# Kernel optimization log

Measured on AMD Instinct MI355X. Metric: run time of the kernel, lower is better.

The kernel has to match this reference:

```python
import jax, jax.numpy as jnp
import numpy as np
from jax import lax

H = 256  # hidden_dim
NDIM = 3
K = 32   # k_neighbors


def sincos_embed(coords, dim, ndim):
    # ContinuousSinCosEmbed: per-coordinate sin/cos features, zero-padded to `dim`.
    dpn = dim // ndim          # channels per coordinate
    half = dpn // 2
    freqs = 1.0 / (10000.0 ** (jnp.arange(half, dtype=coords.dtype) / half))
    ang = coords[..., :, None] * freqs                      # (..., ndim, half)
    emb = jnp.concatenate([jnp.sin(ang), jnp.cos(ang)], -1)  # (..., ndim, 2*half)
    emb = emb.reshape(coords.shape[:-1] + (ndim * 2 * half,))
    pad = dim - ndim * 2 * half
    if pad:
        emb = jnp.concatenate([emb, jnp.zeros(emb.shape[:-1] + (pad,), emb.dtype)], -1)
    return emb


def setup_inputs() -> dict:
    key = jax.random.key(0)
    ks = jax.random.split(key, 8)
    N, S = 50000, 1024
    positions = jax.random.uniform(ks[0], (N, NDIM), dtype=jnp.float32) * 10.0
    supernode_indices = jax.random.randint(ks[1], (S,), 0, N, dtype=jnp.int32)
    g = 1.0 / np.sqrt(H)
    W1 = jax.random.normal(ks[2], (H, H), jnp.float32) * g
    b1 = jnp.zeros((H,), jnp.float32)
    W2 = jax.random.normal(ks[3], (H, H), jnp.float32) * g
    b2 = jnp.zeros((H,), jnp.float32)
    Wp = jax.random.normal(ks[4], (2 * H, H), jnp.float32) * (1.0 / np.sqrt(2 * H))
    bp = jnp.zeros((H,), jnp.float32)
    return {"positions": positions, "supernode_indices": supernode_indices,
            "W1": W1, "b1": b1, "W2": W2, "b2": b2, "Wp": Wp, "bp": bp}


def reference(positions, supernode_indices, W1, b1, W2, b2, Wp, bp):
    # positions: (N, 3); supernode_indices: (S,)
    sup_pos = positions[supernode_indices]                 # (S, 3)
    # kNN neighbor search via dense pairwise squared distances (memory-bound)
    diff = sup_pos[:, None, :] - positions[None, :, :]     # (S, N, 3)
    dist2 = jnp.sum(diff * diff, axis=-1)                  # (S, N)
    _, nbr_idx = lax.top_k(-dist2, K)                      # (S, K)
    nbr_pos = positions[nbr_idx]                           # (S, K, 3)
    # relpos mode: embed (relative position, distance) -> ndim+1 = 4 coords
    rel = sup_pos[:, None, :] - nbr_pos                    # (S, K, 3)
    d = jnp.sqrt(jnp.sum(rel * rel, axis=-1, keepdims=True))  # (S, K, 1)
    rel_feat = jnp.concatenate([rel, d], axis=-1)          # (S, K, 4)
    msg_in = sincos_embed(rel_feat, H, NDIM + 1)           # (S, K, H)
    # message MLP: Dense -> gelu -> Dense
    h = jax.nn.gelu(jnp.einsum('ski,ij->skj', msg_in, W1) + b1)
    msgs = jnp.einsum('ski,ij->skj', h, W2) + b2           # (S, K, H)
    # scatter-reduce: mean over neighbors per supernode
    agg = jnp.mean(msgs, axis=1)                           # (S, H)
    # supernode absolute position embedding, concat, project
    sup_emb = sincos_embed(sup_pos, H, NDIM)               # (S, H)
    feats = jnp.concatenate([sup_emb, agg], axis=-1)       # (S, 2H)
    out = feats @ Wp + bp                                  # (S, H)
    return out[None]                                        # (1, S, H)
```

## Files before the change

### kernel.cpp

```cpp
#include <hip/hip_runtime.h>
#include <hip/hip_bf16.h>
#include <math.h>

typedef short bf16x8 __attribute__((ext_vector_type(8)));
typedef float f32x4  __attribute__((ext_vector_type(4)));

constexpr int   H     = 256;
constexpr int   KNB   = 32;
constexpr int   GC    = 16;
constexpr float HINV  = 1.6f;
constexpr float HCEL  = 0.625f;
constexpr int   SLOTS = 32;
constexpr int   OCAP  = 256;
constexpr int   CAP   = 512;

__device__ __forceinline__ ushort f2bf(float x) {
    unsigned u = __float_as_uint(x);
    u += 0x7FFF + ((u >> 16) & 1);
    return (ushort)(u >> 16);
}

__device__ __forceinline__ float gelu_fast(float x) {
    float u = 0.7978845608028654f * (x + 0.044715f * x * x * x);
    float t = exp2f(-2.885390081777927f * u);
    return x / (1.0f + t);
}

__device__ __forceinline__ int cell_of(float x, float y, float z) {
    int cx = min(GC - 1, max(0, (int)(x * HINV)));
    int cy = min(GC - 1, max(0, (int)(y * HINV)));
    int cz = min(GC - 1, max(0, (int)(z * HINV)));
    return (cz * GC + cy) * GC + cx;
}

__global__ __launch_bounds__(256)
void prep(const float* __restrict__ W1, const float* __restrict__ pos, int N,
          ushort* __restrict__ W1t, float4* __restrict__ pos4s,
          int* __restrict__ origidx, int* __restrict__ cellcnt,
          int* __restrict__ ovfidx, float4* __restrict__ ovfpos) {
    const int b = blockIdx.x;
    if (b < 64) {
        __shared__ float tile[32][33];
        const int ti = b >> 3, tj = b & 7;
        const int r  = threadIdx.x >> 5, c = threadIdx.x & 31;
#pragma unroll
        for (int rr = r; rr < 32; rr += 8)
            tile[rr][c] = W1[(ti * 32 + rr) * H + tj * 32 + c];
        __syncthreads();
#pragma unroll
        for (int rr = r; rr < 32; rr += 8) {
            int j = tj * 32 + rr;
            W1t[j * H + ti * 32 + c] = f2bf(tile[c][rr]);
        }
    } else {
        int i = (b - 64) * 256 + threadIdx.x;
        if (i < N) {
            float x = pos[3 * i], y = pos[3 * i + 1], z = pos[3 * i + 2];
            float4 P = make_float4(x, y, z, 0.f);
            int c = cell_of(x, y, z);
            int slot = atomicAdd(&cellcnt[c], 1);
            if (slot < SLOTS) {
                pos4s[c * SLOTS + slot] = P;
                origidx[c * SLOTS + slot] = i;
            } else {
                int o = atomicAdd(&cellcnt[4096], 1);
                if (o < OCAP) { ovfpos[o] = P; ovfidx[o] = i; }
            }
        }
    }
}

__global__ __launch_bounds__(256, 4)
void fused_knn_mlp(const float* __restrict__ pos,
                   const float4* __restrict__ pos4s,
                   const int* __restrict__ origidx,
                   const int* __restrict__ cellcnt,
                   const int* __restrict__ ovfidx, const float4* __restrict__ ovfpos,
                   const int* __restrict__ supidx,
                   const ushort* __restrict__ W1t, const float* __restrict__ b1,
                   const float* __restrict__ W2, const float* __restrict__ b2,
                   float* __restrict__ featsM)
{
    __shared__ __align__(16) char pool[16384];
    float* amaxd = (float*)pool;
    int*   acnt  = (int*)(pool + 512);
    int*   ccell = (int*)(pool + 1024);
    int*   ccnt  = (int*)(pool + 2048);
    float* cmnd  = (float*)(pool + 3072);
    int*   cpre  = (int*)(pool + 4096);
    float* d2buf = (float*)(pool + 5120);
    int*   obuf  = (int*)(pool + 7168);
    float* pxb   = (float*)(pool + 9216);
    float* pyb   = (float*)(pool + 11264);
    float* pzb   = (float*)(pool + 13312);
    ushort* msg  = (ushort*)pool;
    float*  p2   = (float*)pool;

    __shared__ float rf[KNB][5];
    __shared__ int   selo[KNB];
    __shared__ float hb[H];
    __shared__ int   wsum[4];
    __shared__ float tau2_sh, tau32_sh;
    __shared__ int   cnt_sh, ncl;

    const int s    = blockIdx.x;
    const int t    = threadIdx.x;
    const int lane = t & 63;
    const int w    = t >> 6;

    const int sidx = supidx[s];
    const float sx = pos[3 * sidx], sy = pos[3 * sidx + 1], sz = pos[3 * sidx + 2];

    constexpr float L2_10000 = 13.287712379549449f;

    if (t == 0) { ncl = 0; tau2_sh = 301.f; }

    const int scx = min(GC - 1, max(0, (int)(sx * HINV)));
    const int scy = min(GC - 1, max(0, (int)(sy * HINV)));
    const int scz = min(GC - 1, max(0, (int)(sz * HINV)));
    const int ax0 = max(0, scx - 2), ax1 = min(GC - 1, scx + 2);
    const int ay0 = max(0, scy - 2), ay1 = min(GC - 1, scy + 2);
    const int az0 = max(0, scz - 2), az1 = min(GC - 1, scz + 2);
    const int anx = ax1 - ax0 + 1, any_ = ay1 - ay0 + 1, anz = az1 - az0 + 1;
    const int an  = anx * any_ * anz;
    for (int ci = t; ci < an; ci += 256) {
        int X = ax0 + ci % anx, rem = ci / anx;
        int Y = ay0 + rem % any_, Z = az0 + rem / any_;
        int cell = (Z * GC + Y) * GC + X;
        acnt[ci] = min(cellcnt[cell], SLOTS);
        float lx = X * HCEL, ly = Y * HCEL, lz = Z * HCEL;
        float mx = fmaxf(fabsf(sx - lx), fabsf(lx + HCEL - sx));
        float my = fmaxf(fabsf(sy - ly), fabsf(ly + HCEL - sy));
        float mz = fmaxf(fabsf(sz - lz), fabsf(lz + HCEL - sz));
        amaxd[ci] = mx * mx + my * my + mz * mz;
    }

    {
        float se = 0.f;
        if (t < 252) {
            int c  = t / 84;
            int rr = t - c * 84;
            int f  = (rr < 42) ? rr : rr - 42;
            float coord = (c == 0) ? sx : ((c == 1) ? sy : sz);
            float ang = coord * exp2f(-(float)f * (L2_10000 / 42.f));
            se = (rr < 42) ? __sinf(ang) : __cosf(ang);
        }
        featsM[s * (2 * H) + t] = se;
    }
    __syncthreads();
    for (int ci = t; ci < an; ci += 256) {
        float myv = amaxd[ci];
        int Sc = 0;
        for (int j = 0; j < an; j++) {
            bool less = (amaxd[j] < myv) || (amaxd[j] == myv && j < ci);
            Sc += less ? acnt[j] : 0;
        }
        if (Sc < KNB && KNB <= Sc + acnt[ci]) tau2_sh = myv;
    }
    __syncthreads();
    const float tau2 = tau2_sh;
    const float R2 = tau2 + 1e-3f;
    const float R  = sqrtf(R2);
    if (t == 0) tau32_sh = R2;

    const int bx0 = max(0, (int)floorf((sx - R) * HINV));
    const int bx1 = min(GC - 1, (int)floorf((sx + R) * HINV));
    const int by0 = max(0, (int)floorf((sy - R) * HINV));
    const int by1 = min(GC - 1, (int)floorf((sy + R) * HINV));
    const int bz0 = max(0, (int)floorf((sz - R) * HINV));
    const int bz1 = min(GC - 1, (int)floorf((sz + R) * HINV));
    const bool inwin = (bx0 >= ax0 && bx1 <= ax1 && by0 >= ay0 && by1 <= ay1 &&
                        bz0 >= az0 && bz1 <= az1);
    if (inwin) {
        for (int ci = t; ci < an; ci += 256) {
            int cn = acnt[ci];
            if (cn == 0) continue;
            int X = ax0 + ci % anx, rem = ci / anx;
            int Y = ay0 + rem % any_, Z = az0 + rem / any_;
            float lx = X * HCEL, ly = Y * HCEL, lz = Z * HCEL;
            float ddx = fmaxf(fmaxf(lx - sx, sx - (lx + HCEL)), 0.f);
            float ddy = fmaxf(fmaxf(ly - sy, sy - (ly + HCEL)), 0.f);
            float ddz = fmaxf(fmaxf(lz - sz, sz - (lz + HCEL)), 0.f);
            float mnd = ddx * ddx + ddy * ddy + ddz * ddz;
            if (mnd > R2) continue;
            int p1 = (amaxd[ci] <= tau2) ? 1 : 0;
            int cell = (Z * GC + Y) * GC + X;
            int sl = atomicAdd(&ncl, 1);
            if (sl < 256) { ccell[sl] = cell; ccnt[sl] = cn | (p1 << 8); cmnd[sl] = mnd; }
        }
    } else {
        const int nbx = bx1 - bx0 + 1, nby = by1 - by0 + 1, nbz = bz1 - bz0 + 1;
        const int ncb = nbx * nby * nbz;
        for (int ci = t; ci < ncb; ci += 256) {
            int X = bx0 + ci % nbx, rem = ci / nbx;
            int Y = by0 + rem % nby, Z = bz0 + rem / nby;
            float lx = X * HCEL, ly = Y * HCEL, lz = Z * HCEL;
            float ddx = fmaxf(fmaxf(lx - sx, sx - (lx + HCEL)), 0.f);
            float ddy = fmaxf(fmaxf(ly - sy, sy - (ly + HCEL)), 0.f);
            float ddz = fmaxf(fmaxf(lz - sz, sz - (lz + HCEL)), 0.f);
            float mnd = ddx * ddx + ddy * ddy + ddz * ddz;
            if (mnd > R2) continue;
            int cell = (Z * GC + Y) * GC + X;
            int cn = min(cellcnt[cell], SLOTS);
            if (cn == 0) continue;
            float mx = fmaxf(fabsf(sx - lx), fabsf(lx + HCEL - sx));
            float my = fmaxf(fabsf(sy - ly), fabsf(ly + HCEL - sy));
            float mz = fmaxf(fabsf(sz - lz), fabsf(lz + HCEL - sz));
            float amx = mx * mx + my * my + mz * mz;
            int p1 = (amx <= tau2) ? 1 : 0;
            int sl = atomicAdd(&ncl, 1);
            if (sl < 256) { ccell[sl] = cell; ccnt[sl] = cn | (p1 << 8); cmnd[sl] = mnd; }
        }
    }
    __syncthreads();
    const int nclc = min(ncl, 256);

    auto build_prefix = [&](int phase, float tlim) -> int {
        int v = 0;
        if (t < nclc) {
            int cc = ccnt[t];
            int cn = cc & 0xff;
            int p1 = cc >> 8;
            v = (phase == 1) ? (p1 ? cn : 0)
                             : ((!p1 && cmnd[t] <= tlim) ? cn : 0);
        }
#pragma unroll
        for (int off = 1; off < 64; off <<= 1) {
            int x = __shfl_up(v, off);
            if (lane >= off) v += x;
        }
        if (lane == 63) wsum[w] = v;
        __syncthreads();
        int add = 0;
#pragma unroll
        for (int j = 0; j < 4; j++) if (j < w) add += wsum[j];
        v += add;
        cpre[t] = v;
        __syncthreads();
        return cpre[255];
    };
    auto bsearch = [&](int j) -> int {
        int lo = 0;
#pragma unroll
        for (int st = 128; st; st >>= 1) {
            int nlo = lo + st;
            if (nlo <= 256 && cpre[nlo - 1] <= j) lo = nlo;
        }
        return lo;
    };

    const int tot1 = build_prefix(1, 0.f);
    const int M1 = min(tot1, CAP);
    for (int j0 = 0; j0 < M1; j0 += 256) {
        int j = j0 + t;
        if (j < M1) {
            int lo = bsearch(j);
            int off = j - (lo ? cpre[lo - 1] : 0);
            int u = ccell[lo] * SLOTS + off;
            float4 P = pos4s[u];
            float dx = sx - P.x, dy = sy - P.y, dz = sz - P.z;
            d2buf[j] = dx * dx + dy * dy + dz * dz;
            obuf[j]  = origidx[u];
            pxb[j] = P.x; pyb[j] = P.y; pzb[j] = P.z;
        }
    }
    const int Mp1 = (M1 + 3) & ~3;
    for (int u = M1 + t; u < Mp1; u += 256) { d2buf[u] = INFINITY; obuf[u] = 0x7fffffff; }
    if (t == 0) cnt_sh = M1;
    __syncthreads();

    for (int u = t; u < M1; u += 256) {
        float myv = d2buf[u];
        int   myo = obuf[u];
        int rank = 0;
        for (int v2 = 0; v2 < Mp1; v2 += 4) {
            float4 dv = *(const float4*)&d2buf[v2];
            int4   iv = *(const int4*)&obuf[v2];
            rank += (dv.x < myv) || (dv.x == myv && iv.x < myo);
            rank += (dv.y < myv) || (dv.y == myv && iv.y < myo);
            rank += (dv.z < myv) || (dv.z == myv && iv.z < myo);
            rank += (dv.w < myv) || (dv.w == myv && iv.w < myo);
        }
        if (rank == KNB - 1) tau32_sh = myv;
    }
    __syncthreads();
    const float tau32 = tau32_sh;

    const int tot2 = build_prefix(2, tau32);
    for (int j0 = 0; j0 < tot2; j0 += 256) {
        int j = j0 + t;
        bool pass = false; float pd2 = 0.f; int po = 0; float qx = 0, qy = 0, qz = 0;
        if (j < tot2) {
            int lo = bsearch(j);
            int off = j - (lo ? cpre[lo - 1] : 0);
            int u = ccell[lo] * SLOTS + off;
            float4 P = pos4s[u];
            float dx = sx - P.x, dy = sy - P.y, dz = sz - P.z;
            pd2 = dx * dx + dy * dy + dz * dz;
            if (pd2 <= tau32) { pass = true; po = origidx[u]; qx = P.x; qy = P.y; qz = P.z; }
        }
        unsigned long long m = __ballot(pass);
        if (m) {
            int ldr = __ffsll(m) - 1;
            int base = 0;
            if (lane == ldr) base = atomicAdd(&cnt_sh, __popcll(m));
            base = __shfl(base, ldr);
            if (pass) {
                int slp = base + __popcll(m & ((1ull << lane) - 1ull));
                if (slp < CAP) {
                    d2buf[slp] = pd2; obuf[slp] = po;
                    pxb[slp] = qx; pyb[slp] = qy; pzb[slp] = qz;
                }
            }
        }
    }
    {
        int no = min(cellcnt[4096], OCAP);
        for (int j = t; j < no; j += 256) {
            float4 P = ovfpos[j];
            float dx = sx - P.x, dy = sy - P.y, dz = sz - P.z;
            float pd2 = dx * dx + dy * dy + dz * dz;
            if (pd2 <= tau32) {
                int slp = atomicAdd(&cnt_sh, 1);
                if (slp < CAP) {
                    d2buf[slp] = pd2; obuf[slp] = ovfidx[j];
                    pxb[slp] = P.x; pyb[slp] = P.y; pzb[slp] = P.z;
                }
            }
        }
    }
    __syncthreads();
    const int M = min(cnt_sh, CAP);
    const int Mpad = (M + 3) & ~3;
    for (int u = M + t; u < Mpad; u += 256) { d2buf[u] = INFINITY; obuf[u] = 0x7fffffff; }
    __syncthreads();

    for (int u = t; u < M; u += 256) {
        float myv = d2buf[u];
        int   myo = obuf[u];
        int rank = 0;
        for (int v2 = 0; v2 < Mpad; v2 += 4) {
            float4 dv = *(const float4*)&d2buf[v2];
            int4   iv = *(const int4*)&obuf[v2];
            rank += (dv.x < myv) || (dv.x == myv && iv.x < myo);
            rank += (dv.y < myv) || (dv.y == myv && iv.y < myo);
            rank += (dv.z < myv) || (dv.z == myv && iv.z < myo);
            rank += (dv.w < myv) || (dv.w == myv && iv.w < myo);
        }
        if (rank < KNB) selo[rank] = u;
    }
    __syncthreads();
    if (t < KNB) {
        int u = selo[t];
        float rx = sx - pxb[u], ry = sy - pyb[u], rz = sz - pzb[u];
        float dd = sqrtf(d2buf[u]);
        rf[t][0] = rx; rf[t][1] = ry; rf[t][2] = rz; rf[t][3] = dd;
    }
    __syncthreads();

#pragma unroll
    for (int n = 0; n < 16; n++) {
        int item = t + n * 256;
        int f = item & 31;
        int c = (item >> 5) & 3;
        int k = item >> 7;
        float ang = rf[k][c] * exp2f(-(float)f * (L2_10000 / 32.f));
        int swz = (k & 7) << 3;
        msg[((k << 8) | (c * 64 + f))      ^ swz] = f2bf(__sinf(ang));
        msg[((k << 8) | (c * 64 + 32 + f)) ^ swz] = f2bf(__cosf(ang));
    }
    __syncthreads();

    {
        const int lr = lane & 15;
        const int lg = lane >> 4;
        f32x4 acc[4][2];
#pragma unroll
        for (int mt = 0; mt < 4; mt++)
#pragma unroll
            for (int nt = 0; nt < 2; nt++) acc[mt][nt] = (f32x4){0, 0, 0, 0};
#pragma unroll
        for (int kk = 0; kk < 8; kk++) {
            const int i0 = kk * 32 + lg * 8;
            const int swz = (lr & 7) << 3;
            bf16x8 b0  = *(const bf16x8*)(msg + ((( lr       << 8) | i0) ^ swz));
            bf16x8 b1v = *(const bf16x8*)(msg + ((((lr + 16) << 8) | i0) ^ swz));
#pragma unroll
            for (int mt = 0; mt < 4; mt++) {
                bf16x8 a = *(const bf16x8*)(W1t + ((64 * w + 16 * mt + lr) << 8) + i0);
                acc[mt][0] = __builtin_amdgcn_mfma_f32_16x16x32_bf16(a, b0,  acc[mt][0], 0, 0, 0);
                acc[mt][1] = __builtin_amdgcn_mfma_f32_16x16x32_bf16(a, b1v, acc[mt][1], 0, 0, 0);
            }
        }
        float part[16];
#pragma unroll
        for (int mt = 0; mt < 4; mt++)
#pragma unroll
            for (int r = 0; r < 4; r++) {
                int j = 64 * w + 16 * mt + 4 * lg + r;
                float bj = b1[j];
                part[mt * 4 + r] = gelu_fast(acc[mt][0][r] + bj) + gelu_fast(acc[mt][1][r] + bj);
            }
#pragma unroll
        for (int off = 1; off < 16; off <<= 1)
#pragma unroll
            for (int u = 0; u < 16; u++)
                part[u] += __shfl_xor(part[u], off);
        if (lr == 0) {
#pragma unroll
            for (int u = 0; u < 16; u++) {
                int mt = u >> 2, r = u & 3;
                hb[64 * w + 16 * mt + 4 * lg + r] = part[u] * (1.0f / 32.0f);
            }
        }
    }
    __syncthreads();

    {
        const int g  = t >> 6;
        const int j4 = (t & 63) * 4;
        const int ib = g * 64;
        float4 a = {0.f, 0.f, 0.f, 0.f};
        for (int i = 0; i < 64; i++) {
            float hv = hb[ib + i];
            float4 wv = *(const float4*)&W2[(ib + i) * H + j4];
            a.x = fmaf(hv, wv.x, a.x); a.y = fmaf(hv, wv.y, a.y);
            a.z = fmaf(hv, wv.z, a.z); a.w = fmaf(hv, wv.w, a.w);
        }
        *(float4*)&p2[g * 256 + j4] = a;
    }
    __syncthreads();
    {
        float agg = p2[t] + p2[256 + t] + p2[512 + t] + p2[768 + t] + b2[t];
        featsM[s * (2 * H) + H + t] = agg;
    }
}

__global__ __launch_bounds__(256)
void gemm_bias(const float* __restrict__ A, const float* __restrict__ B,
               const float* __restrict__ bias, float* __restrict__ C,
               int K, int N, int ldc)
{
    __shared__ float As[32][36];
    __shared__ float Bs[32][36];
    const int t  = threadIdx.x;
    const int bm = blockIdx.x, bn = blockIdx.y;
    const int tx = t & 15, ty = t >> 4;
    const int lr = t >> 3, lc = (t & 7) * 4;

    float acc[2][2] = {{0.f, 0.f}, {0.f, 0.f}};

    for (int kk = 0; kk < K; kk += 32) {
        float4 av = *(const float4*)&A[(bm * 32 + lr) * K + kk + lc];
        float4 bv = *(const float4*)&B[(kk + lr) * N + bn * 32 + lc];
        *(float4*)&As[lr][lc] = av;
        *(float4*)&Bs[lr][lc] = bv;
        __syncthreads();
#pragma unroll
        for (int k = 0; k < 32; k++) {
            float a0 = As[2 * ty][k], a1 = As[2 * ty + 1][k];
            float2 b01 = *(const float2*)&Bs[k][2 * tx];
            acc[0][0] += a0 * b01.x; acc[0][1] += a0 * b01.y;
            acc[1][0] += a1 * b01.x; acc[1][1] += a1 * b01.y;
        }
        __syncthreads();
    }
#pragma unroll
    for (int u = 0; u < 2; u++) {
        int row = bm * 32 + 2 * ty + u;
        int col = bn * 32 + 2 * tx;
        C[row * ldc + col]     = acc[u][0] + bias[col];
        C[row * ldc + col + 1] = acc[u][1] + bias[col + 1];
    }
}

extern "C" void kernel_launch(void* const* d_in, const int* in_sizes, int n_in,
                              void* d_out, int out_size, void* d_ws, size_t ws_size,
                              hipStream_t stream) {
    const float* pos = (const float*)d_in[0];
    const int*   sup = (const int*)d_in[1];
    const float* W1  = (const float*)d_in[2];
    const float* b1  = (const float*)d_in[3];
    const float* W2  = (const float*)d_in[4];
    const float* b2  = (const float*)d_in[5];
    const float* Wp  = (const float*)d_in[6];
    const float* bp  = (const float*)d_in[7];

    const int N = in_sizes[0] / 3;
    const int S = in_sizes[1];
    float* out = (float*)d_out;

    char* ws = (char*)d_ws;
    ushort* W1t     = (ushort*)ws;
    float4* pos4s   = (float4*)(ws + (128 << 10));
    int*    origidx = (int*)(ws + (2176 << 10));
    int*    cellcnt = (int*)(ws + (2688 << 10));
    int*    ovfidx  = (int*)(ws + (2708 << 10));
    float4* ovfpos  = (float4*)(ws + (2712 << 10));
    float*  featsM  = (float*)(ws + (2720 << 10));

    hipMemsetAsync(cellcnt, 0, 4097 * sizeof(int), stream);
    prep<<<64 + (N + 255) / 256, 256, 0, stream>>>(W1, pos, N, W1t, pos4s,
                                                   origidx, cellcnt, ovfidx, ovfpos);
    fused_knn_mlp<<<S, 256, 0, stream>>>(pos, pos4s, origidx, cellcnt,
                                         ovfidx, ovfpos, sup,
                                         W1t, b1, W2, b2, featsM);
    gemm_bias<<<dim3(S / 32, H / 32), 256, 0, stream>>>(featsM, Wp, bp, out,
                                                        2 * H, H, H);
}
```

Before: 83.66 us.

## Double threads per block in fused kNN-MLP kernel and split MLP across eight waves

Raises the fused kNN+MLP kernel from 256 to 512 threads per supernode block. Strided loops become single-pass guarded branches, since 512 threads cover every candidate-list size. The W1 MFMA stage now gives each of eight waves 32 output rows instead of 64, and the W2 stage splits into eight partial sums reduced at the end. This aims to shorten each block's serial critical path. The cost is more barrier participants, a larger p2 scratch buffer and a tighter register budget from the (512, 8) launch bounds, which could cause spills.

```diff
diff --git a/kernel.cpp b/kernel.cpp
--- a/kernel.cpp
+++ b/kernel.cpp
@@ -7,6 +7,7 @@
 
 constexpr int   H     = 256;
 constexpr int   KNB   = 32;
+constexpr int   TPB   = 512;
 constexpr int   GC    = 16;
 constexpr float HINV  = 1.6f;
 constexpr float HCEL  = 0.625f;
@@ -70,7 +71,7 @@
     }
 }
 
-__global__ __launch_bounds__(256, 4)
+__global__ __launch_bounds__(TPB, 8)
 void fused_knn_mlp(const float* __restrict__ pos,
                    const float4* __restrict__ pos4s,
                    const int* __restrict__ origidx,
@@ -123,7 +124,8 @@
     const int az0 = max(0, scz - 2), az1 = min(GC - 1, scz + 2);
     const int anx = ax1 - ax0 + 1, any_ = ay1 - ay0 + 1, anz = az1 - az0 + 1;
     const int an  = anx * any_ * anz;
-    for (int ci = t; ci < an; ci += 256) {
+    if (t < an) {
+        int ci = t;
         int X = ax0 + ci % anx, rem = ci / anx;
         int Y = ay0 + rem % any_, Z = az0 + rem / any_;
         int cell = (Z * GC + Y) * GC + X;
@@ -135,7 +137,7 @@
         amaxd[ci] = mx * mx + my * my + mz * mz;
     }
 
-    {
+    if (t < 256) {
         float se = 0.f;
         if (t < 252) {
             int c  = t / 84;
@@ -148,7 +150,8 @@
         featsM[s * (2 * H) + t] = se;
     }
     __syncthreads();
-    for (int ci = t; ci < an; ci += 256) {
+    if (t < an) {
+        int ci = t;
         float myv = amaxd[ci];
         int Sc = 0;
         for (int j = 0; j < an; j++) {
@@ -172,26 +175,29 @@
     const bool inwin = (bx0 >= ax0 && bx1 <= ax1 && by0 >= ay0 && by1 <= ay1 &&
                         bz0 >= az0 && bz1 <= az1);
     if (inwin) {
-        for (int ci = t; ci < an; ci += 256) {
+        if (t < an) {
+            int ci = t;
             int cn = acnt[ci];
-            if (cn == 0) continue;
-            int X = ax0 + ci % anx, rem = ci / anx;
-            int Y = ay0 + rem % any_, Z = az0 + rem / any_;
-            float lx = X * HCEL, ly = Y * HCEL, lz = Z * HCEL;
-            float ddx = fmaxf(fmaxf(lx - sx, sx - (lx + HCEL)), 0.f);
-            float ddy = fmaxf(fmaxf(ly - sy, sy - (ly + HCEL)), 0.f);
-            float ddz = fmaxf(fmaxf(lz - sz, sz - (lz + HCEL)), 0.f);
-            float mnd = ddx * ddx + ddy * ddy + ddz * ddz;
-            if (mnd > R2) continue;
-            int p1 = (amaxd[ci] <= tau2) ? 1 : 0;
-            int cell = (Z * GC + Y) * GC + X;
-            int sl = atomicAdd(&ncl, 1);
-            if (sl < 256) { ccell[sl] = cell; ccnt[sl] = cn | (p1 << 8); cmnd[sl] = mnd; }
+            if (cn > 0) {
+                int X = ax0 + ci % anx, rem = ci / anx;
+                int Y = ay0 + rem % any_, Z = az0 + rem / any_;
+                float lx = X * HCEL, ly = Y * HCEL, lz = Z * HCEL;
+                float ddx = fmaxf(fmaxf(lx - sx, sx - (lx + HCEL)), 0.f);
+                float ddy = fmaxf(fmaxf(ly - sy, sy - (ly + HCEL)), 0.f);
+                float ddz = fmaxf(fmaxf(lz - sz, sz - (lz + HCEL)), 0.f);
+                float mnd = ddx * ddx + ddy * ddy + ddz * ddz;
+                if (mnd <= R2) {
+                    int p1 = (amaxd[ci] <= tau2) ? 1 : 0;
+                    int cell = (Z * GC + Y) * GC + X;
+                    int sl = atomicAdd(&ncl, 1);
+                    if (sl < 256) { ccell[sl] = cell; ccnt[sl] = cn | (p1 << 8); cmnd[sl] = mnd; }
+                }
+            }
         }
     } else {
         const int nbx = bx1 - bx0 + 1, nby = by1 - by0 + 1, nbz = bz1 - bz0 + 1;
         const int ncb = nbx * nby * nbz;
-        for (int ci = t; ci < ncb; ci += 256) {
+        for (int ci = t; ci < ncb; ci += TPB) {
             int X = bx0 + ci % nbx, rem = ci / nbx;
             int Y = by0 + rem % nby, Z = bz0 + rem / nby;
             float lx = X * HCEL, ly = Y * HCEL, lz = Z * HCEL;
@@ -217,25 +223,28 @@
 
     auto build_prefix = [&](int phase, float tlim) -> int {
         int v = 0;
-        if (t < nclc) {
-            int cc = ccnt[t];
-            int cn = cc & 0xff;
-            int p1 = cc >> 8;
-            v = (phase == 1) ? (p1 ? cn : 0)
-                             : ((!p1 && cmnd[t] <= tlim) ? cn : 0);
-        }
-#pragma unroll
-        for (int off = 1; off < 64; off <<= 1) {
-            int x = __shfl_up(v, off);
-            if (lane >= off) v += x;
-        }
-        if (lane == 63) wsum[w] = v;
+        if (t < 256) {
+            if (t < nclc) {
+                int cc = ccnt[t];
+                int cn = cc & 0xff;
+                int p1 = cc >> 8;
+                v = (phase == 1) ? (p1 ? cn : 0)
+                                 : ((!p1 && cmnd[t] <= tlim) ? cn : 0);
+            }
+#pragma unroll
+            for (int off = 1; off < 64; off <<= 1) {
+                int x = __shfl_up(v, off);
+                if (lane >= off) v += x;
+            }
+            if (lane == 63) wsum[w] = v;
+        }
         __syncthreads();
-        int add = 0;
-#pragma unroll
-        for (int j = 0; j < 4; j++) if (j < w) add += wsum[j];
-        v += add;
-        cpre[t] = v;
+        if (t < 256) {
+            int add = 0;
+#pragma unroll
+            for (int j = 0; j < 4; j++) if (j < w) add += wsum[j];
+            cpre[t] = v + add;
+        }
         __syncthreads();
         return cpre[255];
     };
@@ -251,25 +260,24 @@
 
     const int tot1 = build_prefix(1, 0.f);
     const int M1 = min(tot1, CAP);
-    for (int j0 = 0; j0 < M1; j0 += 256) {
-        int j = j0 + t;
-        if (j < M1) {
-            int lo = bsearch(j);
-            int off = j - (lo ? cpre[lo - 1] : 0);
-            int u = ccell[lo] * SLOTS + off;
-            float4 P = pos4s[u];
-            float dx = sx - P.x, dy = sy - P.y, dz = sz - P.z;
-            d2buf[j] = dx * dx + dy * dy + dz * dz;
-            obuf[j]  = origidx[u];
-            pxb[j] = P.x; pyb[j] = P.y; pzb[j] = P.z;
-        }
+    if (t < M1) {
+        int j = t;
+        int lo = bsearch(j);
+        int off = j - (lo ? cpre[lo - 1] : 0);
+        int u = ccell[lo] * SLOTS + off;
+        float4 P = pos4s[u];
+        float dx = sx - P.x, dy = sy - P.y, dz = sz - P.z;
+        d2buf[j] = dx * dx + dy * dy + dz * dz;
+        obuf[j]  = origidx[u];
+        pxb[j] = P.x; pyb[j] = P.y; pzb[j] = P.z;
     }
     const int Mp1 = (M1 + 3) & ~3;
-    for (int u = M1 + t; u < Mp1; u += 256) { d2buf[u] = INFINITY; obuf[u] = 0x7fffffff; }
+    if (M1 + t < Mp1) { d2buf[M1 + t] = INFINITY; obuf[M1 + t] = 0x7fffffff; }
     if (t == 0) cnt_sh = M1;
     __syncthreads();
 
-    for (int u = t; u < M1; u += 256) {
+    if (t < M1) {
+        int u = t;
         float myv = d2buf[u];
         int   myo = obuf[u];
         int rank = 0;
@@ -287,7 +295,7 @@
     const float tau32 = tau32_sh;
 
     const int tot2 = build_prefix(2, tau32);
-    for (int j0 = 0; j0 < tot2; j0 += 256) {
+    for (int j0 = 0; j0 < tot2; j0 += TPB) {
         int j = j0 + t;
         bool pass = false; float pd2 = 0.f; int po = 0; float qx = 0, qy = 0, qz = 0;
         if (j < tot2) {
@@ -316,7 +324,7 @@
     }
     {
         int no = min(cellcnt[4096], OCAP);
-        for (int j = t; j < no; j += 256) {
+        for (int j = t; j < no; j += TPB) {
             float4 P = ovfpos[j];
             float dx = sx - P.x, dy = sy - P.y, dz = sz - P.z;
             float pd2 = dx * dx + dy * dy + dz * dz;
@@ -332,10 +340,11 @@
     __syncthreads();
     const int M = min(cnt_sh, CAP);
     const int Mpad = (M + 3) & ~3;
-    for (int u = M + t; u < Mpad; u += 256) { d2buf[u] = INFINITY; obuf[u] = 0x7fffffff; }
-    __syncthreads();
-
-    for (int u = t; u < M; u += 256) {
+    if (M + t < Mpad) { d2buf[M + t] = INFINITY; obuf[M + t] = 0x7fffffff; }
+    __syncthreads();
+
+    if (t < M) {
+        int u = t;
         float myv = d2buf[u];
         int   myo = obuf[u];
         int rank = 0;
@@ -359,8 +368,8 @@
     __syncthreads();
 
 #pragma unroll
-    for (int n = 0; n < 16; n++) {
-        int item = t + n * 256;
+    for (int n = 0; n < 8; n++) {
+        int item = t + n * TPB;
         int f = item & 31;
         int c = (item >> 5) & 3;
         int k = item >> 7;
@@ -374,64 +383,65 @@
     {
         const int lr = lane & 15;
         const int lg = lane >> 4;
-        f32x4 acc[4][2];
-#pragma unroll
-        for (int mt = 0; mt < 4; mt++)
-#pragma unroll
-            for (int nt = 0; nt < 2; nt++) acc[mt][nt] = (f32x4){0, 0, 0, 0};
+        f32x4 acc00 = {0,0,0,0}, acc01 = {0,0,0,0};
+        f32x4 acc10 = {0,0,0,0}, acc11 = {0,0,0,0};
 #pragma unroll
         for (int kk = 0; kk < 8; kk++) {
             const int i0 = kk * 32 + lg * 8;
+            bf16x8 a0 = *(const bf16x8*)(W1t + ((32 * w      + lr) << 8) + i0);
+            bf16x8 a1 = *(const bf16x8*)(W1t + ((32 * w + 16 + lr) << 8) + i0);
             const int swz = (lr & 7) << 3;
             bf16x8 b0  = *(const bf16x8*)(msg + ((( lr       << 8) | i0) ^ swz));
             bf16x8 b1v = *(const bf16x8*)(msg + ((((lr + 16) << 8) | i0) ^ swz));
-#pragma unroll
-            for (int mt = 0; mt < 4; mt++) {
-                bf16x8 a = *(const bf16x8*)(W1t + ((64 * w + 16 * mt + lr) << 8) + i0);
-                acc[mt][0] = __builtin_amdgcn_mfma_f32_16x16x32_bf16(a, b0,  acc[mt][0], 0, 0, 0);
-                acc[mt][1] = __builtin_amdgcn_mfma_f32_16x16x32_bf16(a, b1v, acc[mt][1], 0, 0, 0);
-            }
-        }
-        float part[16];
-#pragma unroll
-        for (int mt = 0; mt < 4; mt++)
+            acc00 = __builtin_amdgcn_mfma_f32_16x16x32_bf16(a0, b0,  acc00, 0, 0, 0);
+            acc01 = __builtin_amdgcn_mfma_f32_16x16x32_bf16(a0, b1v, acc01, 0, 0, 0);
+            acc10 = __builtin_amdgcn_mfma_f32_16x16x32_bf16(a1, b0,  acc10, 0, 0, 0);
+            acc11 = __builtin_amdgcn_mfma_f32_16x16x32_bf16(a1, b1v, acc11, 0, 0, 0);
+        }
+        float part[8];
+#pragma unroll
+        for (int mm = 0; mm < 2; mm++)
 #pragma unroll
             for (int r = 0; r < 4; r++) {
-                int j = 64 * w + 16 * mt + 4 * lg + r;
+                int j = 32 * w + 16 * mm + 4 * lg + r;
                 float bj = b1[j];
-                part[mt * 4 + r] = gelu_fast(acc[mt][0][r] + bj) + gelu_fast(acc[mt][1][r] + bj);
+                float h0 = (mm == 0 ? acc00[r] : acc10[r]) + bj;
+                float h1 = (mm == 0 ? acc01[r] : acc11[r]) + bj;
+                part[mm * 4 + r] = gelu_fast(h0) + gelu_fast(h1);
             }
 #pragma unroll
         for (int off = 1; off < 16; off <<= 1)
 #pragma unroll
-            for (int u = 0; u < 16; u++)
+            for (int u = 0; u < 8; u++)
                 part[u] += __shfl_xor(part[u], off);
         if (lr == 0) {
 #pragma unroll
-            for (int u = 0; u < 16; u++) {
-                int mt = u >> 2, r = u & 3;
-                hb[64 * w + 16 * mt + 4 * lg + r] = part[u] * (1.0f / 32.0f);
+            for (int u = 0; u < 8; u++) {
+                int mm = u >> 2, r = u & 3;
+                hb[32 * w + 16 * mm + 4 * lg + r] = part[u] * (1.0f / 32.0f);
             }
         }
     }
     __syncthreads();
 
     {
-        const int g  = t >> 6;
-        const int j4 = (t & 63) * 4;
-        const int ib = g * 64;
+        const int j4 = lane * 4;
+        const int ib = w * 32;
         float4 a = {0.f, 0.f, 0.f, 0.f};
-        for (int i = 0; i < 64; i++) {
+#pragma unroll 4
+        for (int i = 0; i < 32; i++) {
             float hv = hb[ib + i];
             float4 wv = *(const float4*)&W2[(ib + i) * H + j4];
             a.x = fmaf(hv, wv.x, a.x); a.y = fmaf(hv, wv.y, a.y);
             a.z = fmaf(hv, wv.z, a.z); a.w = fmaf(hv, wv.w, a.w);
         }
-        *(float4*)&p2[g * 256 + j4] = a;
-    }
-    __syncthreads();
-    {
-        float agg = p2[t] + p2[256 + t] + p2[512 + t] + p2[768 + t] + b2[t];
+        *(float4*)&p2[w * 256 + j4] = a;
+    }
+    __syncthreads();
+    if (t < 256) {
+        float agg = b2[t];
+#pragma unroll
+        for (int g = 0; g < 8; g++) agg += p2[g * 256 + t];
         featsM[s * (2 * H) + H + t] = agg;
     }
 }
@@ -502,7 +512,7 @@
     hipMemsetAsync(cellcnt, 0, 4097 * sizeof(int), stream);
     prep<<<64 + (N + 255) / 256, 256, 0, stream>>>(W1, pos, N, W1t, pos4s,
                                                    origidx, cellcnt, ovfidx, ovfpos);
-    fused_knn_mlp<<<S, 256, 0, stream>>>(pos, pos4s, origidx, cellcnt,
+    fused_knn_mlp<<<S, TPB, 0, stream>>>(pos, pos4s, origidx, cellcnt,
                                          ovfidx, ovfpos, sup,
                                          W1t, b1, W2, b2, featsM);
     gemm_bias<<<dim3(S / 32, H / 32), 256, 0, stream>>>(featsM, Wp, bp, out,
```

Measured after the change: 83.01 us. About the same (-0.8%).
